# Kernel tuning notes

Hardware: AMD Instinct MI355X
Metric: run time of the kernel (lower is better)

The kernel has to match this reference:

```python
import jax, jax.numpy as jnp
import numpy as np

B, N, E, P, PH, H = 4, 512, 768, 64, 32, 8
D = E // H  # 96
FFN = 3072

def _ln(x, g, b, eps=1e-5):
    mu = jnp.mean(x, axis=-1, keepdims=True)
    var = jnp.mean((x - mu) ** 2, axis=-1, keepdims=True)
    return (x - mu) * jax.lax.rsqrt(var + eps) * g + b

def setup_inputs() -> dict:
    key = jax.random.key(0)
    ks = iter(jax.random.split(key, 80))
    def f(*s):
        return jax.random.normal(next(ks), s, jnp.float32) * 0.02
    ones = lambda *s: jnp.ones(s, jnp.float32)
    zeros = lambda *s: jnp.zeros(s, jnp.float32)
    return {
        'x': jax.random.normal(next(ks), (B, N, E), jnp.float32),
        'pair': jax.random.normal(next(ks), (B, N, N, P), jnp.float32) * 0.5,
        'attn_mask': zeros(B, 1, N, N),
        'op_mask': ones(B, N, 1),
        'op_norm': ones(1) / N,
        'nlist': jax.random.randint(next(ks), (B, N, 64), 0, N),
        'wq': f(E, E), 'wk': f(E, E), 'wv': f(E, E),
        'wg': f(E, E), 'bg': zeros(E),
        'wo': f(E, E), 'bo': zeros(E),
        'ln_pair_g': ones(P), 'ln_pair_b': zeros(P),
        'wb': f(H, P), 'bb': zeros(H),
        'ln_attn_g': ones(E), 'ln_attn_b': zeros(E),
        'ln_ffn_g': ones(E), 'ln_ffn_b': zeros(E),
        'w_ffn1': f(FFN, E), 'b_ffn1': zeros(FFN),
        'w_ffn2': f(E, FFN), 'b_ffn2': zeros(E),
        'ln_opm_g': ones(E), 'ln_opm_b': zeros(E),
        'w_opm_in': f(2 * PH, E), 'b_opm_in': zeros(2 * PH),
        'w_opm_out': f(P, PH * PH), 'b_opm_out': zeros(P),
        'ln_tm_g': ones(P), 'ln_tm_b': zeros(P),
        'w_tm_abp': f(2 * PH, P), 'b_tm_abp': zeros(2 * PH),
        'w_tm_abg': f(2 * PH, P), 'b_tm_abg': zeros(2 * PH),
        'w_tm_g': f(P, P), 'b_tm_g': zeros(P),
        'w_tm_z': f(P, PH), 'b_tm_z': zeros(P),
        'ln_tmo_g': ones(PH), 'ln_tmo_b': zeros(PH),
        'ln_pffn_g': ones(P), 'ln_pffn_b': zeros(P),
        'w_pffn1': f(P, P), 'b_pffn1': zeros(P),
        'w_pffn2': f(P, P), 'b_pffn2': zeros(P),
    }

def _forward(x, pair, attn_mask, op_mask, op_norm, wq, wk, wv, wg, bg, wo, bo,
             ln_pair_g, ln_pair_b, wb, bb, ln_attn_g, ln_attn_b,
             ln_ffn_g, ln_ffn_b, w_ffn1, b_ffn1, w_ffn2, b_ffn2,
             ln_opm_g, ln_opm_b, w_opm_in, b_opm_in, w_opm_out, b_opm_out,
             ln_tm_g, ln_tm_b, w_tm_abp, b_tm_abp, w_tm_abg, b_tm_abg,
             w_tm_g, b_tm_g, w_tm_z, b_tm_z, ln_tmo_g, ln_tmo_b,
             ln_pffn_g, ln_pffn_b, w_pffn1, b_pffn1, w_pffn2, b_pffn2):
    Bx, Nx, _ = x.shape
    # --- gated pair-bias self-attention (pre-LN, eval mode: dropout = identity) ---
    h = _ln(x, ln_attn_g, ln_attn_b)
    pn = _ln(pair, ln_pair_g, ln_pair_b)               # AtomAttention pair LayerNorm
    bias = jnp.einsum('bijp,hp->bhij', pn, wb) + bb[None, :, None, None]
    q = (h @ wq.T).reshape(Bx, Nx, H, D).transpose(0, 2, 1, 3) * (D ** -0.5)
    k = (h @ wk.T).reshape(Bx, Nx, H, D).transpose(0, 2, 1, 3)
    v = (h @ wv.T).reshape(Bx, Nx, H, D).transpose(0, 2, 1, 3)
    attn = jax.nn.softmax(jnp.einsum('bhid,bhjd->bhij', q, k) + attn_mask + bias, axis=-1)
    o = jnp.einsum('bhij,bhjd->bhid', attn, v).transpose(0, 2, 1, 3).reshape(Bx, Nx, E)
    o = jax.nn.sigmoid(h @ wg.T + bg) * o              # sigmoid output gate
    x = x + (o @ wo.T + bo)
    # --- atom transition MLP ---
    h = _ln(x, ln_ffn_g, ln_ffn_b)
    x = x + (jax.nn.gelu(h @ w_ffn1.T + b_ffn1, approximate=False) @ w_ffn2.T + b_ffn2)
    # --- OuterProduct pair update (fused: avoids [B,N,N,PH*PH] intermediate) ---
    h = _ln(x, ln_opm_g, ln_opm_b)
    ab = (h @ w_opm_in.T + b_opm_in) * op_mask
    a_o, b_o = jnp.split(ab, 2, axis=-1)               # each [B,N,PH]
    z = jnp.einsum('bid,bje,pde->bijp', a_o, b_o, w_opm_out.reshape(P, PH, PH)) + b_opm_out
    pair = pair + z * op_norm
    # --- triangle multiplication ---
    zp = _ln(pair, ln_tm_g, ln_tm_b)
    gpr = zp @ w_tm_g.T + b_tm_g                       # gate (no sigmoid, matches source)
    ab = (zp @ w_tm_abp.T + b_tm_abp) * jax.nn.sigmoid(zp @ w_tm_abg.T + b_tm_abg)
    a_t, b_t = jnp.split(ab, 2, axis=-1)               # each [B,N,N,PH]
    t = jnp.einsum('bijh,bkjh->bhik', a_t, b_t) + jnp.einsum('bjih,bjkh->bhik', a_t, b_t)
    t = _ln(t.transpose(0, 2, 3, 1), ln_tmo_g, ln_tmo_b) @ w_tm_z.T + b_tm_z
    pair = pair + gpr * t
    # --- pair transition MLP ---
    zp = _ln(pair, ln_pffn_g, ln_pffn_b)
    pair = pair + (jax.nn.gelu(zp @ w_pffn1.T + b_pffn1, approximate=False) @ w_pffn2.T + b_pffn2)
    return x, pair

def reference(x, pair, attn_mask, op_mask, op_norm, nlist, wq, wk, wv, wg, bg, wo, bo,
              ln_pair_g, ln_pair_b, wb, bb, ln_attn_g, ln_attn_b,
              ln_ffn_g, ln_ffn_b, w_ffn1, b_ffn1, w_ffn2, b_ffn2,
              ln_opm_g, ln_opm_b, w_opm_in, b_opm_in, w_opm_out, b_opm_out,
              ln_tm_g, ln_tm_b, w_tm_abp, b_tm_abp, w_tm_abg, b_tm_abg,
              w_tm_g, b_tm_g, w_tm_z, b_tm_z, ln_tmo_g, ln_tmo_b,
              ln_pffn_g, ln_pffn_b, w_pffn1, b_pffn1, w_pffn2, b_pffn2):
    del nlist  # accepted by the torch module but unused in the math
    return _forward(x, pair, attn_mask, op_mask, op_norm, wq, wk, wv, wg, bg, wo, bo,
                    ln_pair_g, ln_pair_b, wb, bb, ln_attn_g, ln_attn_b,
                    ln_ffn_g, ln_ffn_b, w_ffn1, b_ffn1, w_ffn2, b_ffn2,
                    ln_opm_g, ln_opm_b, w_opm_in, b_opm_in, w_opm_out, b_opm_out,
                    ln_tm_g, ln_tm_b, w_tm_abp, b_tm_abp, w_tm_abg, b_tm_abg,
                    w_tm_g, b_tm_g, w_tm_z, b_tm_z, ln_tmo_g, ln_tmo_b,
                    ln_pffn_g, ln_pffn_b, w_pffn1, b_pffn1, w_pffn2, b_pffn2)
```

## Files before the change

### kernel.cpp

```cpp
#include <hip/hip_runtime.h>
#include <hip/hip_bf16.h>
#include <math.h>

#define Nn 512
#define Ee 768
#define Pp 64
#define PHh 32
#define Hh 8
#define Dd 96
#define NNe 262144
#define LNEPS 1e-5f

typedef __attribute__((ext_vector_type(8))) short bf8;
typedef __attribute__((ext_vector_type(4))) short bf4;
typedef __attribute__((ext_vector_type(4))) float f32x4;
#define MFMA(a,b,c) __builtin_amdgcn_mfma_f32_16x16x32_bf16(a,b,c,0,0,0)

__device__ __forceinline__ short f2bf(float f) {
  __bf16 h = (__bf16)f;
  return __builtin_bit_cast(short, h);
}
__device__ __forceinline__ float bf2f(short s) {
  unsigned u = ((unsigned)(unsigned short)s) << 16;
  return __builtin_bit_cast(float, u);
}

__device__ __forceinline__ float wave_red_sum(float v) {
#pragma unroll
  for (int off = 32; off > 0; off >>= 1) v += __shfl_xor(v, off);
  return v;
}
__device__ __forceinline__ float gelu_exact(float v) {
  return 0.5f * v * (1.f + erff(v * 0.70710678118654752f));
}
__device__ __forceinline__ float sigmoidf_(float v) {
  return 1.f / (1.f + __expf(-v));
}
__device__ __forceinline__ float gelu_fast(float v) {
  return v / (1.f + __expf(-1.702f * v));
}

__global__ __launch_bounds__(256) void castw_kernel(
    const float* __restrict__ wq, const float* __restrict__ wk,
    const float* __restrict__ wv, const float* __restrict__ wg,
    const float* __restrict__ wo, const float* __restrict__ f1,
    const float* __restrict__ f2, const float* __restrict__ wop,
    const float* __restrict__ wb, const float* __restrict__ abp,
    const float* __restrict__ abg, const float* __restrict__ wtg,
    const float* __restrict__ wtz, const float* __restrict__ p1,
    const float* __restrict__ p2,
    short* __restrict__ dst, float qs) {
  long i = (long)blockIdx.x * 256 + threadIdx.x;
  float v;
  if (i < 589824) v = wq[i] * qs;
  else if (i < 1179648) v = wk[i - 589824];
  else if (i < 1769472) v = wv[i - 1179648];
  else if (i < 2359296) v = wg[i - 1769472];
  else if (i < 2949120) v = wo[i - 2359296];
  else if (i < 5308416) v = f1[i - 2949120];
  else if (i < 7667712) v = f2[i - 5308416];
  else if (i < 7716864) v = wop[i - 7667712];
  else if (i < 7717376) v = wb[i - 7716864];
  else if (i < 7721472) v = abp[i - 7717376];
  else if (i < 7725568) v = abg[i - 7721472];
  else if (i < 7729664) v = wtg[i - 7725568];
  else if (i < 7731712) v = wtz[i - 7729664];
  else if (i < 7735808) v = p1[i - 7731712];
  else if (i < 7739904) v = p2[i - 7735808];
  else return;
  dst[i] = f2bf(v);
}

__global__ __launch_bounds__(256) void ln_bf_kernel(const float* __restrict__ in,
                                                    short* __restrict__ out,
                                                    const float* __restrict__ gam,
                                                    const float* __restrict__ bet, int C) {
  int row = blockIdx.x;
  const float* xr = in + (long)row * C;
  short* yr = out + (long)row * C;
  float s = 0.f, ss = 0.f;
  for (int c = threadIdx.x; c < C; c += 256) { float v = xr[c]; s += v; ss += v * v; }
  s = wave_red_sum(s); ss = wave_red_sum(ss);
  __shared__ float sm[4][2];
  int wv = threadIdx.x >> 6, lane = threadIdx.x & 63;
  if (lane == 0) { sm[wv][0] = s; sm[wv][1] = ss; }
  __syncthreads();
  float ts = sm[0][0] + sm[1][0] + sm[2][0] + sm[3][0];
  float tss = sm[0][1] + sm[1][1] + sm[2][1] + sm[3][1];
  float mu = ts / C;
  float var = tss / C - mu * mu;
  float rs = rsqrtf(var + LNEPS);
  for (int c = threadIdx.x; c < C; c += 256) {
    float v = xr[c];
    yr[c] = f2bf((v - mu) * rs * gam[c] + bet[c]);
  }
}

__global__ __launch_bounds__(256) void gemm_bf(
    const short* __restrict__ A, int lda, long asB, long asH,
    const short* __restrict__ Bm, int ldb, long bsB, long bsH,
    float* __restrict__ outF, int ldf, long fsB, long fsH,
    short* __restrict__ outB, int ldob,
    const float* __restrict__ resid, int ldr, long rsB, long rsH,
    const float* __restrict__ bias,
    int M, int N, int K, int act, int vtrans, int Hdim) {
  int bz = blockIdx.z, bb = bz / Hdim, hh = bz % Hdim;
  A += bb * asB + hh * asH;
  Bm += bb * bsB + hh * bsH;
  if (outF) outF += bb * fsB + hh * fsH;
  if (outB) outB += bb * fsB + hh * fsH;
  if (resid) resid += bb * rsB + hh * rsH;
  __shared__ __align__(16) short As[64 * 72];
  __shared__ __align__(16) short Bs[64 * 72];
  int m0 = blockIdx.y * 64, n0 = blockIdx.x * 64;
  int tid = threadIdx.x;
  int wv = tid >> 6, lane = tid & 63;
  int wr = wv >> 1, wc = wv & 1;
  int lhi = lane >> 4, llo = lane & 15;
  int r4 = tid >> 2, c8 = (tid & 3) * 8;
  f32x4 acc[2][2] = {};
  for (int k0 = 0; k0 < K; k0 += 64) {
    *(bf8*)&As[r4 * 72 + c8] = *(const bf8*)(A + (long)(m0 + r4) * lda + k0 + c8);
    *(bf8*)&As[r4 * 72 + 32 + c8] =
        *(const bf8*)(A + (long)(m0 + r4) * lda + k0 + 32 + c8);
    bf8 bv0 = {}, bv1 = {};
    if (n0 + r4 < N) {
      bv0 = *(const bf8*)(Bm + (long)(n0 + r4) * ldb + k0 + c8);
      bv1 = *(const bf8*)(Bm + (long)(n0 + r4) * ldb + k0 + 32 + c8);
    }
    *(bf8*)&Bs[r4 * 72 + c8] = bv0;
    *(bf8*)&Bs[r4 * 72 + 32 + c8] = bv1;
    __syncthreads();
#pragma unroll
    for (int ks = 0; ks < 2; ++ks) {
      bf8 a0 = *(const bf8*)&As[(wr * 32 + llo) * 72 + ks * 32 + lhi * 8];
      bf8 a1 = *(const bf8*)&As[(wr * 32 + 16 + llo) * 72 + ks * 32 + lhi * 8];
      bf8 b0 = *(const bf8*)&Bs[(wc * 32 + llo) * 72 + ks * 32 + lhi * 8];
      bf8 b1 = *(const bf8*)&Bs[(wc * 32 + 16 + llo) * 72 + ks * 32 + lhi * 8];
      acc[0][0] = MFMA(a0, b0, acc[0][0]);
      acc[0][1] = MFMA(a0, b1, acc[0][1]);
      acc[1][0] = MFMA(a1, b0, acc[1][0]);
      acc[1][1] = MFMA(a1, b1, acc[1][1]);
    }
    __syncthreads();
  }
#pragma unroll
  for (int mi = 0; mi < 2; ++mi) {
    int gmb = m0 + wr * 32 + mi * 16 + lhi * 4;
#pragma unroll
    for (int ni = 0; ni < 2; ++ni) {
      int gn = n0 + wc * 32 + ni * 16 + llo;
      if (gn >= N) continue;
      float bv = bias ? bias[gn] : 0.f;
      float vr[4];
#pragma unroll
      for (int r = 0; r < 4; ++r) {
        float v = acc[mi][ni][r] + bv;
        if (resid) {
          float rv = resid[(long)(gmb + r) * ldr + gn];
          if (act == 2) v = sigmoidf_(rv) * acc[mi][ni][r];
          else v += rv;
        }
        if (act == 1) v = gelu_exact(v);
        vr[r] = v;
      }
      if (outF) {
#pragma unroll
        for (int r = 0; r < 4; ++r) outF[(long)(gmb + r) * ldf + gn] = vr[r];
      }
      if (outB) {
        if (vtrans) {
          bf4 pk;
#pragma unroll
          for (int r = 0; r < 4; ++r) pk[r] = f2bf(vr[r]);
          *(bf4*)(outB + ((long)((gmb >> 9) * 768 + gn) * 512 + (gmb & 511))) = pk;
        } else {
#pragma unroll
          for (int r = 0; r < 4; ++r) outB[(long)(gmb + r) * ldob + gn] = f2bf(vr[r]);
        }
      }
    }
  }
}

__global__ __launch_bounds__(256) void gemm_qkvg(
    const short* __restrict__ A, const short* __restrict__ W,
    short* __restrict__ q_bf, short* __restrict__ k_bf,
    short* __restrict__ vT_bf, float* __restrict__ gb,
    const float* __restrict__ bg) {
  __shared__ __align__(16) short As[128 * 40];
  __shared__ __align__(16) short Bs[128 * 40];
  int m0 = blockIdx.y * 128, n0 = blockIdx.x * 128;
// ... 393 lines not shown
#pragma unroll
    for (int mi = 0; mi < 2; ++mi)
#pragma unroll
      for (int r = 0; r < 4; ++r) { float v = x[mi][ni][r]; s += v; ss += v * v; }
    int e = wc * 32 + ni * 16 + llo;
    spS[grp][e][wr * 4 + lhi] = s;
    spQ[grp][e][wr * 4 + lhi] = ss;
  }
  __syncthreads();
  float mu1[2], rs1[2];
#pragma unroll
  for (int ni = 0; ni < 2; ++ni) {
    int e = wc * 32 + ni * 16 + llo;
    float s = 0.f, q2 = 0.f;
#pragma unroll
    for (int k = 0; k < 8; ++k) { s += spS[grp][e][k]; q2 += spQ[grp][e][k]; }
    float mu = s * 0.015625f, var = q2 * 0.015625f - mu * mu;
    mu1[ni] = mu; rs1[ni] = rsqrtf(var + LNEPS);
  }
#pragma unroll
  for (int mi = 0; mi < 2; ++mi) {
    f32x4 gv = *(const f32x4*)(gam + chb + mi * 16);
    f32x4 bv = *(const f32x4*)(bet + chb + mi * 16);
#pragma unroll
    for (int ni = 0; ni < 2; ++ni) {
      int e = wc * 32 + ni * 16 + llo;
      bf4 pk;
#pragma unroll
      for (int r = 0; r < 4; ++r)
        pk[r] = f2bf((x[mi][ni][r] - mu1[ni]) * rs1[ni] * gv[r] + bv[r]);
      *(bf4*)&Zb[grp][e * 72 + chb + mi * 16] = pk;
    }
  }
  __syncthreads();
  f32x4 ap[2][2] = {};
  f32x4 ag[2][2] = {};
#pragma unroll
  for (int ks = 0; ks < 2; ++ks) {
    bf8 z0 = *(const bf8*)&Zb[grp][(wr * 32 + llo) * 72 + ks * 32 + fc];
    bf8 z1 = *(const bf8*)&Zb[grp][(wr * 32 + 16 + llo) * 72 + ks * 32 + fc];
    bf8 p0 = *(const bf8*)&Wp[(wc * 32 + llo) * 72 + ks * 32 + fc];
    bf8 p1 = *(const bf8*)&Wp[(wc * 32 + 16 + llo) * 72 + ks * 32 + fc];
    bf8 g0 = *(const bf8*)&Wg[(wc * 32 + llo) * 72 + ks * 32 + fc];
    bf8 g1 = *(const bf8*)&Wg[(wc * 32 + 16 + llo) * 72 + ks * 32 + fc];
    ap[0][0] = MFMA(z0, p0, ap[0][0]);
    ap[0][1] = MFMA(z0, p1, ap[0][1]);
    ap[1][0] = MFMA(z1, p0, ap[1][0]);
    ap[1][1] = MFMA(z1, p1, ap[1][1]);
    ag[0][0] = MFMA(z0, g0, ag[0][0]);
    ag[0][1] = MFMA(z0, g1, ag[0][1]);
    ag[1][0] = MFMA(z1, g0, ag[1][0]);
    ag[1][1] = MFMA(z1, g1, ag[1][1]);
  }
#pragma unroll
  for (int mi = 0; mi < 2; ++mi) {
    int elemb = wr * 32 + mi * 16 + lhi * 4;
#pragma unroll
    for (int ni = 0; ni < 2; ++ni) {
      int ch = wc * 32 + ni * 16 + llo;
      float bp = b_abp[ch], bg = b_abg[ch];
      bf4 pack;
#pragma unroll
      for (int r = 0; r < 4; ++r)
        pack[r] = f2bf((ap[mi][ni][r] + bp) * sigmoidf_(ag[mi][ni][r] + bg));
      short* dst = (ch < 32) ? (aN + (long)ch * NNe) : (bN + (long)(ch - 32) * NNe);
      *(bf4*)(dst + ebase + elemb) = pack;
    }
  }
}

__global__ __launch_bounds__(512) void tm_tri_mfma(const short* __restrict__ aN4,
                                                   const short* __restrict__ bN4,
                                                   short* __restrict__ t4) {
  int lin = blockIdx.z * 16 + blockIdx.y * 4 + blockIdx.x;
  int vid = (lin & 7) * 256 + (lin >> 3);
  int hh = vid >> 4;
  int b = hh >> 5, h = hh & 31;
  int rem = vid & 15;
  int i0 = (rem >> 2) * 128, k0 = (rem & 3) * 128;
  const short* A = aN4 + (long)b * 8388608 + (long)h * NNe;
  const short* B = bN4 + (long)b * 8388608 + (long)h * NNe;
  __shared__ __align__(16) short A1[128 * 40];
  __shared__ __align__(16) short B1[128 * 40];
  __shared__ __align__(16) short A2[128 * 40];
  __shared__ __align__(16) short B2[128 * 40];
  int tid = threadIdx.x;
  int wv = tid >> 6, lane = tid & 63;
  int wr = wv >> 2, wc = wv & 3;
  int lhi = lane >> 4, llo = lane & 15;
  int r1 = tid >> 2, cp = (tid & 3) * 8;
  int s2 = tid >> 5, cg = (tid & 31) * 4;
  f32x4 acc[4][2] = {};
  for (int j0 = 0; j0 < 512; j0 += 32) {
    *(bf8*)&A1[r1 * 40 + cp] = *(const bf8*)(A + (long)(i0 + r1) * 512 + j0 + cp);
    *(bf8*)&B1[r1 * 40 + cp] = *(const bf8*)(B + (long)(k0 + r1) * 512 + j0 + cp);
    bf4 va0 = *(const bf4*)(A + (long)(j0 + 2 * s2) * 512 + i0 + cg);
    bf4 va1 = *(const bf4*)(A + (long)(j0 + 2 * s2 + 1) * 512 + i0 + cg);
    bf4 vb0 = *(const bf4*)(B + (long)(j0 + 2 * s2) * 512 + k0 + cg);
    bf4 vb1 = *(const bf4*)(B + (long)(j0 + 2 * s2 + 1) * 512 + k0 + cg);
#pragma unroll
    for (int q = 0; q < 4; ++q) {
      unsigned pa = (unsigned)(unsigned short)va0[q] |
                    ((unsigned)(unsigned short)va1[q] << 16);
      unsigned pb = (unsigned)(unsigned short)vb0[q] |
                    ((unsigned)(unsigned short)vb1[q] << 16);
      *(unsigned*)&A2[(cg + q) * 40 + 2 * s2] = pa;
      *(unsigned*)&B2[(cg + q) * 40 + 2 * s2] = pb;
    }
    __syncthreads();
    bf8 bfr[2], dfr[2];
#pragma unroll
    for (int ni = 0; ni < 2; ++ni) {
      bfr[ni] = *(const bf8*)&B1[(wc * 32 + ni * 16 + llo) * 40 + lhi * 8];
      dfr[ni] = *(const bf8*)&B2[(wc * 32 + ni * 16 + llo) * 40 + lhi * 8];
    }
#pragma unroll
    for (int mi = 0; mi < 4; ++mi) {
      bf8 a = *(const bf8*)&A1[(wr * 64 + mi * 16 + llo) * 40 + lhi * 8];
      acc[mi][0] = MFMA(a, bfr[0], acc[mi][0]);
      acc[mi][1] = MFMA(a, bfr[1], acc[mi][1]);
    }
#pragma unroll
    for (int mi = 0; mi < 4; ++mi) {
      bf8 c = *(const bf8*)&A2[(wr * 64 + mi * 16 + llo) * 40 + lhi * 8];
      acc[mi][0] = MFMA(c, dfr[0], acc[mi][0]);
      acc[mi][1] = MFMA(c, dfr[1], acc[mi][1]);
    }
    __syncthreads();
  }
  short* tp = t4 + (long)b * 8388608 + (long)h * NNe;
#pragma unroll
  for (int mi = 0; mi < 4; ++mi)
#pragma unroll
    for (int ni = 0; ni < 2; ++ni) {
      int row = i0 + wr * 64 + mi * 16 + lhi * 4;
      int col = k0 + wc * 32 + ni * 16 + llo;
#pragma unroll
      for (int r = 0; r < 4; ++r) tp[(long)(row + r) * 512 + col] = f2bf(acc[mi][ni][r]);
    }
}

__global__ __launch_bounds__(512) void upd_pffn_fused(
    const float* __restrict__ pin, float* __restrict__ pout,
    const short* __restrict__ t4,
    const short* __restrict__ Tb, const short* __restrict__ bo_bf,
    const float* __restrict__ b_out, const float* __restrict__ op_norm,
    const float* __restrict__ g_tm, const float* __restrict__ b_tm,
    const short* __restrict__ wg_a, const float* __restrict__ b_g,
    const short* __restrict__ wz_a, const float* __restrict__ b_z,
    const float* __restrict__ g_tmo, const float* __restrict__ b_tmo,
    const float* __restrict__ g_pf, const float* __restrict__ b_pf,
    const short* __restrict__ w1_a, const float* __restrict__ b1,
    const short* __restrict__ w2_a, const float* __restrict__ b2) {
  __shared__ __align__(16) short Zb[2][64 * 72];
  __shared__ __align__(16) short Tlb[2][64 * 40];
  __shared__ __align__(16) short Wbuf[64 * 72];
  __shared__ __align__(16) short Wzb[64 * 36];
  __shared__ float spS[2][64][9];
  __shared__ float spQ[2][64][9];
  __shared__ float spB[2][4][2][72];
  int tid = threadIdx.x;
  int grp = tid >> 8;
  int t = tid & 255;
  long e0 = (long)blockIdx.x * 128 + grp * 64;
  int bbt = (int)(e0 >> 18);
  long el = e0 & (NNe - 1);
  long growT = e0 >> 9;
  int jt = (int)((e0 >> 6) & 7);
  int wv = t >> 6, lane = t & 63;
  int wr = wv >> 1, wc = wv & 1;
  int lhi = lane >> 4, llo = lane & 15;
  int chb = wr * 32 + lhi * 4;
  int fc = lhi * 8;
  int fr0 = wr * 32 + llo, fr1 = fr0 + 16;
  int br0 = wc * 32 + llo, br1 = br0 + 16;
  int r0 = tid >> 3, c0 = (tid & 7) * 8;
  bf8 w1r, w2r;
  {
    *(bf8*)&Wbuf[r0 * 72 + c0] = *(const bf8*)(wg_a + r0 * 64 + c0);
    w1r = *(const bf8*)(w1_a + r0 * 64 + c0);
    w2r = *(const bf8*)(w2_a + r0 * 64 + c0);
    int rz = tid >> 3, cz = (tid & 7) * 4;
    *(bf4*)&Wzb[rz * 36 + cz] = *(const bf4*)(wz_a + rz * 32 + cz);
  }
  f32x4 x[2][2];
#pragma unroll
  for (int mi = 0; mi < 2; ++mi)
#pragma unroll
    for (int ni = 0; ni < 2; ++ni)
      x[mi][ni] = *(const f32x4*)(pin + (e0 + wc * 32 + ni * 16 + llo) * 64 +
                                  chb + mi * 16);
  {
    f32x4 acc[2][2] = {};
    bf8 a0 = *(const bf8*)(Tb + growT * 2048 + (long)fr0 * 32 + fc);
    bf8 a1 = *(const bf8*)(Tb + growT * 2048 + (long)fr1 * 32 + fc);
    bf8 b0 = *(const bf8*)(bo_bf + ((long)bbt * 512 + jt * 64 + br0) * 32 + fc);
    bf8 b1 = *(const bf8*)(bo_bf + ((long)bbt * 512 + jt * 64 + br1) * 32 + fc);
    acc[0][0] = MFMA(a0, b0, acc[0][0]);
    acc[0][1] = MFMA(a0, b1, acc[0][1]);
    acc[1][0] = MFMA(a1, b0, acc[1][0]);
    acc[1][1] = MFMA(a1, b1, acc[1][1]);
    float nrm = op_norm[0];
#pragma unroll
    for (int mi = 0; mi < 2; ++mi) {
      f32x4 bo4 = *(const f32x4*)(b_out + chb + mi * 16);
#pragma unroll
      for (int ni = 0; ni < 2; ++ni)
#pragma unroll
        for (int r = 0; r < 4; ++r)
          x[mi][ni][r] += (acc[mi][ni][r] + bo4[r]) * nrm;
    }
  }
#pragma unroll
  for (int ni = 0; ni < 2; ++ni) {
    float s = 0.f, ss = 0.f;
#pragma unroll
    for (int mi = 0; mi < 2; ++mi)
#pragma unroll
      for (int r = 0; r < 4; ++r) { float v = x[mi][ni][r]; s += v; ss += v * v; }
    int e = wc * 32 + ni * 16 + llo;
    spS[grp][e][wr * 4 + lhi] = s;
    spQ[grp][e][wr * 4 + lhi] = ss;
  }
  const short* t_in = t4 + (long)bbt * 8388608;
  int te = t & 63, tq = t >> 6;
  float tt[8];
  {
    float sB = 0.f, ssB = 0.f;
#pragma unroll
    for (int k = 0; k < 8; ++k) {
      float v = bf2f(t_in[(long)(tq * 8 + k) * NNe + el + te]);
      tt[k] = v; sB += v; ssB += v * v;
    }
    spB[grp][tq][0][te] = sB; spB[grp][tq][1][te] = ssB;
  }
  __syncthreads();
  {
    float ts = spB[grp][0][0][te] + spB[grp][1][0][te] + spB[grp][2][0][te] +
               spB[grp][3][0][te];
    float tss = spB[grp][0][1][te] + spB[grp][1][1][te] + spB[grp][2][1][te] +
                spB[grp][3][1][te];
    float mu = ts * 0.03125f, var = tss * 0.03125f - mu * mu;
    float rs = rsqrtf(var + LNEPS);
    bf8 pk;
#pragma unroll
    for (int k = 0; k < 8; ++k) {
      int c = tq * 8 + k;
      pk[k] = f2bf((tt[k] - mu) * rs * g_tmo[c] + b_tmo[c]);
    }
    *(bf8*)&Tlb[grp][te * 40 + tq * 8] = pk;
  }
  float mu1[2], rs1[2];
#pragma unroll
  for (int ni = 0; ni < 2; ++ni) {
    int e = wc * 32 + ni * 16 + llo;
    float s = 0.f, q2 = 0.f;
#pragma unroll
    for (int k = 0; k < 8; ++k) { s += spS[grp][e][k]; q2 += spQ[grp][e][k]; }
    float mu = s * 0.015625f, var = q2 * 0.015625f - mu * mu;
    mu1[ni] = mu; rs1[ni] = rsqrtf(var + LNEPS);
  }
#pragma unroll
  for (int mi = 0; mi < 2; ++mi) {
    f32x4 gv = *(const f32x4*)(g_tm + chb + mi * 16);
    f32x4 bv = *(const f32x4*)(b_tm + chb + mi * 16);
#pragma unroll
    for (int ni = 0; ni < 2; ++ni) {
      int e = wc * 32 + ni * 16 + llo;
      bf4 pk;
#pragma unroll
      for (int r = 0; r < 4; ++r)
        pk[r] = f2bf((x[mi][ni][r] - mu1[ni]) * rs1[ni] * gv[r] + bv[r]);
      *(bf4*)&Zb[grp][e * 72 + chb + mi * 16] = pk;
    }
  }
  __syncthreads();
  f32x4 accg[2][2] = {};
  f32x4 accz[2][2] = {};
#pragma unroll
  for (int ks = 0; ks < 2; ++ks) {
    bf8 a0 = *(const bf8*)&Wbuf[fr0 * 72 + ks * 32 + fc];
    bf8 a1 = *(const bf8*)&Wbuf[fr1 * 72 + ks * 32 + fc];
    bf8 z0 = *(const bf8*)&Zb[grp][br0 * 72 + ks * 32 + fc];
    bf8 z1 = *(const bf8*)&Zb[grp][br1 * 72 + ks * 32 + fc];
    accg[0][0] = MFMA(a0, z0, accg[0][0]);
    accg[0][1] = MFMA(a0, z1, accg[0][1]);
    accg[1][0] = MFMA(a1, z0, accg[1][0]);
    accg[1][1] = MFMA(a1, z1, accg[1][1]);
  }
  {
    bf8 a0 = *(const bf8*)&Wzb[fr0 * 36 + fc];
    bf8 a1 = *(const bf8*)&Wzb[fr1 * 36 + fc];
    bf8 t0 = *(const bf8*)&Tlb[grp][br0 * 40 + fc];
    bf8 t1 = *(const bf8*)&Tlb[grp][br1 * 40 + fc];
    accz[0][0] = MFMA(a0, t0, accz[0][0]);
    accz[0][1] = MFMA(a0, t1, accz[0][1]);
    accz[1][0] = MFMA(a1, t0, accz[1][0]);
    accz[1][1] = MFMA(a1, t1, accz[1][1]);
  }
#pragma unroll
  for (int mi = 0; mi < 2; ++mi) {
    f32x4 bgv = *(const f32x4*)(b_g + chb + mi * 16);
    f32x4 bzv = *(const f32x4*)(b_z + chb + mi * 16);
#pragma unroll
    for (int ni = 0; ni < 2; ++ni)
#pragma unroll
      for (int r = 0; r < 4; ++r)
        x[mi][ni][r] += (accg[mi][ni][r] + bgv[r]) * (accz[mi][ni][r] + bzv[r]);
  }
#pragma unroll
  for (int ni = 0; ni < 2; ++ni) {
    float s = 0.f, ss = 0.f;
#pragma unroll
    for (int mi = 0; mi < 2; ++mi)
#pragma unroll
      for (int r = 0; r < 4; ++r) { float v = x[mi][ni][r]; s += v; ss += v * v; }
    int e = wc * 32 + ni * 16 + llo;
    spS[grp][e][wr * 4 + lhi] = s;
    spQ[grp][e][wr * 4 + lhi] = ss;
  }
  __syncthreads();
  *(bf8*)&Wbuf[r0 * 72 + c0] = w1r;
#pragma unroll
  for (int ni = 0; ni < 2; ++ni) {
    int e = wc * 32 + ni * 16 + llo;
    float s = 0.f, q2 = 0.f;
#pragma unroll
    for (int k = 0; k < 8; ++k) { s += spS[grp][e][k]; q2 += spQ[grp][e][k]; }
    float mu = s * 0.015625f, var = q2 * 0.015625f - mu * mu;
    mu1[ni] = mu; rs1[ni] = rsqrtf(var + LNEPS);
  }
#pragma unroll
  for (int mi = 0; mi < 2; ++mi) {
    f32x4 gv = *(const f32x4*)(g_pf + chb + mi * 16);
    f32x4 bv = *(const f32x4*)(b_pf + chb + mi * 16);
#pragma unroll
    for (int ni = 0; ni < 2; ++ni) {
      int e = wc * 32 + ni * 16 + llo;
      bf4 pk;
#pragma unroll
      for (int r = 0; r < 4; ++r)
        pk[r] = f2bf((x[mi][ni][r] - mu1[ni]) * rs1[ni] * gv[r] + bv[r]);
      *(bf4*)&Zb[grp][e * 72 + chb + mi * 16] = pk;
    }
  }
  __syncthreads();
  f32x4 acc1[2][2] = {};
#pragma unroll
  for (int ks = 0; ks < 2; ++ks) {
    bf8 a0 = *(const bf8*)&Wbuf[fr0 * 72 + ks * 32 + fc];
    bf8 a1 = *(const bf8*)&Wbuf[fr1 * 72 + ks * 32 + fc];
    bf8 z0 = *(const bf8*)&Zb[grp][br0 * 72 + ks * 32 + fc];
    bf8 z1 = *(const bf8*)&Zb[grp][br1 * 72 + ks * 32 + fc];
    acc1[0][0] = MFMA(a0, z0, acc1[0][0]);
    acc1[0][1] = MFMA(a0, z1, acc1[0][1]);
    acc1[1][0] = MFMA(a1, z0, acc1[1][0]);
    acc1[1][1] = MFMA(a1, z1, acc1[1][1]);
  }
  __syncthreads();
  *(bf8*)&Wbuf[r0 * 72 + c0] = w2r;
#pragma unroll
  for (int mi = 0; mi < 2; ++mi) {
    f32x4 bv = *(const f32x4*)(b1 + chb + mi * 16);
#pragma unroll
    for (int ni = 0; ni < 2; ++ni) {
      int e = wc * 32 + ni * 16 + llo;
      bf4 pk;
#pragma unroll
      for (int r = 0; r < 4; ++r) pk[r] = f2bf(gelu_fast(acc1[mi][ni][r] + bv[r]));
      *(bf4*)&Zb[grp][e * 72 + chb + mi * 16] = pk;
    }
  }
  __syncthreads();
  f32x4 acc2[2][2] = {};
#pragma unroll
  for (int ks = 0; ks < 2; ++ks) {
    bf8 a0 = *(const bf8*)&Wbuf[fr0 * 72 + ks * 32 + fc];
    bf8 a1 = *(const bf8*)&Wbuf[fr1 * 72 + ks * 32 + fc];
    bf8 z0 = *(const bf8*)&Zb[grp][br0 * 72 + ks * 32 + fc];
    bf8 z1 = *(const bf8*)&Zb[grp][br1 * 72 + ks * 32 + fc];
    acc2[0][0] = MFMA(a0, z0, acc2[0][0]);
    acc2[0][1] = MFMA(a0, z1, acc2[0][1]);
    acc2[1][0] = MFMA(a1, z0, acc2[1][0]);
    acc2[1][1] = MFMA(a1, z1, acc2[1][1]);
  }
#pragma unroll
  for (int mi = 0; mi < 2; ++mi) {
    f32x4 bv = *(const f32x4*)(b2 + chb + mi * 16);
#pragma unroll
    for (int ni = 0; ni < 2; ++ni) {
#pragma unroll
      for (int r = 0; r < 4; ++r) x[mi][ni][r] += acc2[mi][ni][r] + bv[r];
      *(f32x4*)(pout + (e0 + wc * 32 + ni * 16 + llo) * 64 + chb + mi * 16) =
          x[mi][ni];
    }
  }
}

extern "C" void kernel_launch(void* const* d_in, const int* in_sizes, int n_in,
                              void* d_out, int out_size, void* d_ws, size_t ws_size,
                              hipStream_t stream) {
  const float* x = (const float*)d_in[0];
  const float* pair = (const float*)d_in[1];
  const float* attn_mask = (const float*)d_in[2];
  const float* op_mask = (const float*)d_in[3];
  const float* op_norm = (const float*)d_in[4];
  const float* wq = (const float*)d_in[6];
  const float* wk = (const float*)d_in[7];
  const float* wv_ = (const float*)d_in[8];
  const float* wg = (const float*)d_in[9];
  const float* bg = (const float*)d_in[10];
  const float* wo = (const float*)d_in[11];
  const float* bo = (const float*)d_in[12];
  const float* ln_pair_g = (const float*)d_in[13];
  const float* ln_pair_b = (const float*)d_in[14];
  const float* wb = (const float*)d_in[15];
  const float* bb = (const float*)d_in[16];
  const float* ln_attn_g = (const float*)d_in[17];
  const float* ln_attn_b = (const float*)d_in[18];
  const float* ln_ffn_g = (const float*)d_in[19];
  const float* ln_ffn_b = (const float*)d_in[20];
  const float* w_ffn1 = (const float*)d_in[21];
  const float* b_ffn1 = (const float*)d_in[22];
  const float* w_ffn2 = (const float*)d_in[23];
  const float* b_ffn2 = (const float*)d_in[24];
  const float* ln_opm_g = (const float*)d_in[25];
  const float* ln_opm_b = (const float*)d_in[26];
  const float* w_opm_in = (const float*)d_in[27];
  const float* b_opm_in = (const float*)d_in[28];
  const float* w_opm_out = (const float*)d_in[29];
  const float* b_opm_out = (const float*)d_in[30];
  const float* ln_tm_g = (const float*)d_in[31];
  const float* ln_tm_b = (const float*)d_in[32];
  const float* w_tm_abp = (const float*)d_in[33];
  const float* b_tm_abp = (const float*)d_in[34];
  const float* w_tm_abg = (const float*)d_in[35];
  const float* b_tm_abg = (const float*)d_in[36];
  const float* w_tm_g = (const float*)d_in[37];
  const float* b_tm_g = (const float*)d_in[38];
  const float* w_tm_z = (const float*)d_in[39];
  const float* b_tm_z = (const float*)d_in[40];
  const float* ln_tmo_g = (const float*)d_in[41];
  const float* ln_tmo_b = (const float*)d_in[42];
  const float* ln_pffn_g = (const float*)d_in[43];
  const float* ln_pffn_b = (const float*)d_in[44];
  const float* w_pffn1 = (const float*)d_in[45];
  const float* b_pffn1 = (const float*)d_in[46];
  const float* w_pffn2 = (const float*)d_in[47];
  const float* b_pffn2 = (const float*)d_in[48];

  float* ws = (float*)d_ws;
  short* wbf = (short*)ws;
  short* wq_bf = wbf + 0;
  short* wo_bf = wbf + 2359296;
  short* wf1_bf = wbf + 2949120;
  short* wf2_bf = wbf + 5308416;
  short* wop_bf = wbf + 7667712;
  short* wb_a = wbf + 7716864;
  short* wabp_a = wbf + 7717376;
  short* wabg_a = wbf + 7721472;
  short* wtg_a = wbf + 7725568;
  short* wtz_a = wbf + 7729664;
  short* wp1_a = wbf + 7731712;
  short* wp2_a = wbf + 7735808;

  short* h_bf = (short*)(ws + 3869952);
  short* q_bf = (short*)(ws + 4656384);
  short* k_bf = (short*)(ws + 5442816);
  short* vT_bf = (short*)(ws + 6229248);
  float* gb = ws + 7015680;
  short* gb_bf = (short*)(ws + 10161408);
  float* x1b = ws + 10947840;
  short* biasb_bf = (short*)(ws + 12520704);
  short* attn_bf = (short*)(ws + 16715008);
  short* mffn_bf = (short*)(ws + 20909312);
  float* abb = ws + 24055040;
  short* abb_bf = (short*)(ws + 24186112);
  short* Tb_bf = (short*)(ws + 24218880);
  short* aN4 = (short*)(ws + 59870464);
  short* bN4 = (short*)(ws + 76647680);
  short* t4 = (short*)(ws + 93424896);

  float* xo = (float*)d_out;
  float* pair1 = xo + 1572864;

  const float qscale = 0.1020620726159658f;

  castw_kernel<<<30234, 256, 0, stream>>>(wq, wk, wv_, wg, wo, w_ffn1, w_ffn2, w_opm_in,
                                          wb, w_tm_abp, w_tm_abg, w_tm_g, w_tm_z,
                                          w_pffn1, w_pffn2, wbf, qscale);
  ln_bf_kernel<<<2048, 256, 0, stream>>>(x, h_bf, ln_attn_g, ln_attn_b, 768);
  gemm_qkvg<<<dim3(24, 16, 1), 256, 0, stream>>>(h_bf, wq_bf, q_bf, k_bf, vT_bf, gb, bg);
  pair_bias_mfma<<<8192, 512, 0, stream>>>(pair, ln_pair_g, ln_pair_b, wb_a, bb, biasb_bf);
  attn_fused<<<dim3(32, 8, 4), 256, 0, stream>>>(q_bf, k_bf, biasb_bf, attn_mask, attn_bf);
  gemm_bf<<<dim3(2, 8, 32), 256, 0, stream>>>(attn_bf, 512, 2097152, 262144,
                                              vT_bf, 512, 393216, 49152,
                                              nullptr, 0, 393216, 96, gb_bf, 768,
                                              gb, 768, 393216, 96, nullptr,
                                              512, 96, 512, 2, 0, 8);
  gemm128<<<dim3(6, 16, 1), 256, 0, stream>>>(gb_bf, wo_bf, 768, x, bo, x1b);
  ln_bf_kernel<<<2048, 256, 0, stream>>>(x1b, h_bf, ln_ffn_g, ln_ffn_b, 768);
  gemm_ffn1<<<dim3(24, 16, 1), 256, 0, stream>>>(h_bf, wf1_bf, mffn_bf, b_ffn1);
  gemm128<<<dim3(6, 16, 1), 256, 0, stream>>>(mffn_bf, wf2_bf, 3072, x1b, b_ffn2, xo);
  ln_bf_kernel<<<2048, 256, 0, stream>>>(xo, h_bf, ln_opm_g, ln_opm_b, 768);
  gemm_bf<<<dim3(1, 32, 1), 256, 0, stream>>>(h_bf, 768, 0, 0, wop_bf, 768, 0, 0,
                                              abb, 64, 0, 0, nullptr, 0,
                                              nullptr, 0, 0, 0, b_opm_in,
                                              2048, 64, 768, 0, 0, 1);
  opmask_kernel<<<512, 256, 0, stream>>>(abb, op_mask, abb_bf);
  opm_T_kernel<<<dim3(256, 64, 1), dim3(32, 8, 1), 0, stream>>>(abb, w_opm_out, Tb_bf);
  opm_ab_fused<<<dim3(4, 512, 4), 512, 0, stream>>>(
      pair, Tb_bf, abb_bf, b_opm_out, op_norm,
      ln_tm_g, ln_tm_b, wabp_a, b_tm_abp, wabg_a, b_tm_abg, aN4, bN4);
  tm_tri_mfma<<<dim3(4, 4, 128), 512, 0, stream>>>(aN4, bN4, t4);
  upd_pffn_fused<<<8192, 512, 0, stream>>>(
      pair, pair1, t4, Tb_bf, abb_bf, b_opm_out, op_norm,
      ln_tm_g, ln_tm_b, wtg_a, b_tm_g, wtz_a, b_tm_z,
      ln_tmo_g, ln_tmo_b, ln_pffn_g, ln_pffn_b, wp1_a, b_pffn1, wp2_a, b_pffn2);
}
```

Baseline: 867.0 us.

## Restructure pair update kernel so each wave owns 16 edges and skips block barriers

```diff
diff --git a/kernel.cpp b/kernel.cpp
--- a/kernel.cpp
+++ b/kernel.cpp
@@ -38,6 +38,10 @@
 }
 __device__ __forceinline__ float gelu_fast(float v) {
   return v / (1.f + __expf(-1.702f * v));
+}
+__device__ __forceinline__ void wave_fence() {
+  asm volatile("s_waitcnt lgkmcnt(0)" ::: "memory");
+  __builtin_amdgcn_sched_barrier(0);
 }
 
 __global__ __launch_bounds__(256) void castw_kernel(
@@ -737,248 +741,170 @@
     const float* __restrict__ g_pf, const float* __restrict__ b_pf,
     const short* __restrict__ w1_a, const float* __restrict__ b1,
     const short* __restrict__ w2_a, const float* __restrict__ b2) {
-  __shared__ __align__(16) short Zb[2][64 * 72];
-  __shared__ __align__(16) short Tlb[2][64 * 40];
-  __shared__ __align__(16) short Wbuf[64 * 72];
-  __shared__ __align__(16) short Wzb[64 * 36];
-  __shared__ float spS[2][64][9];
-  __shared__ float spQ[2][64][9];
-  __shared__ float spB[2][4][2][72];
+  __shared__ __align__(16) short Wg[64 * 72];
+  __shared__ __align__(16) short Wz[64 * 36];
+  __shared__ __align__(16) short W1s[64 * 72];
+  __shared__ __align__(16) short W2s[64 * 72];
+  __shared__ __align__(16) short Zw[8][16 * 72];
   int tid = threadIdx.x;
-  int grp = tid >> 8;
-  int t = tid & 255;
-  long e0 = (long)blockIdx.x * 128 + grp * 64;
+  int wid = tid >> 6, lane = tid & 63;
+  int llo = lane & 15, lhi = lane >> 4;
+  long e0 = (long)blockIdx.x * 128;
   int bbt = (int)(e0 >> 18);
-  long el = e0 & (NNe - 1);
+  long el = (e0 & (NNe - 1)) + wid * 16 + llo;
+  long elG = e0 + wid * 16 + llo;
   long growT = e0 >> 9;
-  int jt = (int)((e0 >> 6) & 7);
-  int wv = t >> 6, lane = t & 63;
-  int wr = wv >> 1, wc = wv & 1;
-  int lhi = lane >> 4, llo = lane & 15;
-  int chb = wr * 32 + lhi * 4;
-  int fc = lhi * 8;
-  int fr0 = wr * 32 + llo, fr1 = fr0 + 16;
-  int br0 = wc * 32 + llo, br1 = br0 + 16;
-  int r0 = tid >> 3, c0 = (tid & 7) * 8;
-  bf8 w1r, w2r;
+  int jcol = (int)(el & 511);
   {
-    *(bf8*)&Wbuf[r0 * 72 + c0] = *(const bf8*)(wg_a + r0 * 64 + c0);
-    w1r = *(const bf8*)(w1_a + r0 * 64 + c0);
-    w2r = *(const bf8*)(w2_a + r0 * 64 + c0);
-    int rz = tid >> 3, cz = (tid & 7) * 4;
-    *(bf4*)&Wzb[rz * 36 + cz] = *(const bf4*)(wz_a + rz * 32 + cz);
-  }
-  f32x4 x[2][2];
-#pragma unroll
-  for (int mi = 0; mi < 2; ++mi)
-#pragma unroll
-    for (int ni = 0; ni < 2; ++ni)
-      x[mi][ni] = *(const f32x4*)(pin + (e0 + wc * 32 + ni * 16 + llo) * 64 +
-                                  chb + mi * 16);
+    int r0 = tid >> 3, c0 = (tid & 7) * 8, cz = (tid & 7) * 4;
+    *(bf8*)&Wg[r0 * 72 + c0] = *(const bf8*)(wg_a + r0 * 64 + c0);
+    *(bf8*)&W1s[r0 * 72 + c0] = *(const bf8*)(w1_a + r0 * 64 + c0);
+    *(bf8*)&W2s[r0 * 72 + c0] = *(const bf8*)(w2_a + r0 * 64 + c0);
+    *(bf4*)&Wz[r0 * 36 + cz] = *(const bf4*)(wz_a + r0 * 32 + cz);
+  }
+  short* zb = &Zw[wid][0];
+  f32x4 x[4];
+#pragma unroll
+  for (int mo = 0; mo < 4; ++mo)
+    x[mo] = *(const f32x4*)(pin + elG * 64 + mo * 16 + lhi * 4);
+  const short* t_in = t4 + (long)bbt * 8388608;
+  float tt[8];
+#pragma unroll
+  for (int k = 0; k < 8; ++k)
+    tt[k] = bf2f(t_in[(long)(lhi * 8 + k) * NNe + el]);
   {
-    f32x4 acc[2][2] = {};
-    bf8 a0 = *(const bf8*)(Tb + growT * 2048 + (long)fr0 * 32 + fc);
-    bf8 a1 = *(const bf8*)(Tb + growT * 2048 + (long)fr1 * 32 + fc);
-    bf8 b0 = *(const bf8*)(bo_bf + ((long)bbt * 512 + jt * 64 + br0) * 32 + fc);
-    bf8 b1 = *(const bf8*)(bo_bf + ((long)bbt * 512 + jt * 64 + br1) * 32 + fc);
-    acc[0][0] = MFMA(a0, b0, acc[0][0]);
-    acc[0][1] = MFMA(a0, b1, acc[0][1]);
-    acc[1][0] = MFMA(a1, b0, acc[1][0]);
-    acc[1][1] = MFMA(a1, b1, acc[1][1]);
+    bf8 bo_f = *(const bf8*)(bo_bf + ((long)bbt * 512 + jcol) * 32 + lhi * 8);
     float nrm = op_norm[0];
 #pragma unroll
-    for (int mi = 0; mi < 2; ++mi) {
-      f32x4 bo4 = *(const f32x4*)(b_out + chb + mi * 16);
-#pragma unroll
-      for (int ni = 0; ni < 2; ++ni)
-#pragma unroll
-        for (int r = 0; r < 4; ++r)
-          x[mi][ni][r] += (acc[mi][ni][r] + bo4[r]) * nrm;
-    }
-  }
-#pragma unroll
-  for (int ni = 0; ni < 2; ++ni) {
+    for (int mo = 0; mo < 4; ++mo) {
+      bf8 a = *(const bf8*)(Tb + growT * 2048 + (long)(mo * 16 + llo) * 32 + lhi * 8);
+      f32x4 acc = {0.f, 0.f, 0.f, 0.f};
+      acc = MFMA(a, bo_f, acc);
+      f32x4 bo4 = *(const f32x4*)(b_out + mo * 16 + lhi * 4);
+#pragma unroll
+      for (int r = 0; r < 4; ++r) x[mo][r] += (acc[r] + bo4[r]) * nrm;
+    }
+  }
+  {
     float s = 0.f, ss = 0.f;
 #pragma unroll
-    for (int mi = 0; mi < 2; ++mi)
-#pragma unroll
-      for (int r = 0; r < 4; ++r) { float v = x[mi][ni][r]; s += v; ss += v * v; }
-    int e = wc * 32 + ni * 16 + llo;
-    spS[grp][e][wr * 4 + lhi] = s;
-    spQ[grp][e][wr * 4 + lhi] = ss;
-  }
-  const short* t_in = t4 + (long)bbt * 8388608;
-  int te = t & 63, tq = t >> 6;
-  float tt[8];
+    for (int mo = 0; mo < 4; ++mo)
+#pragma unroll
+      for (int r = 0; r < 4; ++r) { float v = x[mo][r]; s += v; ss += v * v; }
+    s += __shfl_xor(s, 16); s += __shfl_xor(s, 32);
+    ss += __shfl_xor(ss, 16); ss += __shfl_xor(ss, 32);
+    float mu = s * 0.015625f, var = ss * 0.015625f - mu * mu;
+    float rs = rsqrtf(var + LNEPS);
+#pragma unroll
+    for (int mo = 0; mo < 4; ++mo) {
+      f32x4 gv = *(const f32x4*)(g_tm + mo * 16 + lhi * 4);
+      f32x4 bv = *(const f32x4*)(b_tm + mo * 16 + lhi * 4);
+      bf4 pk;
+#pragma unroll
+      for (int r = 0; r < 4; ++r)
+        pk[r] = f2bf((x[mo][r] - mu) * rs * gv[r] + bv[r]);
+      *(bf4*)&zb[llo * 72 + mo * 16 + lhi * 4] = pk;
+    }
+  }
+  __syncthreads();
+  f32x4 accg[4] = {};
+#pragma unroll
+  for (int ks = 0; ks < 2; ++ks) {
+    bf8 zf = *(const bf8*)&zb[llo * 72 + ks * 32 + lhi * 8];
+#pragma unroll
+    for (int mo = 0; mo < 4; ++mo) {
+      bf8 a = *(const bf8*)&Wg[(mo * 16 + llo) * 72 + ks * 32 + lhi * 8];
+      accg[mo] = MFMA(a, zf, accg[mo]);
+    }
+  }
+  f32x4 accz[4] = {};
   {
-    float sB = 0.f, ssB = 0.f;
+    float s = 0.f, ss = 0.f;
+#pragma unroll
+    for (int k = 0; k < 8; ++k) { s += tt[k]; ss += tt[k] * tt[k]; }
+    s += __shfl_xor(s, 16); s += __shfl_xor(s, 32);
+    ss += __shfl_xor(ss, 16); ss += __shfl_xor(ss, 32);
+    float mu = s * 0.03125f, var = ss * 0.03125f - mu * mu;
+    float rs = rsqrtf(var + LNEPS);
+    bf8 tf;
 #pragma unroll
     for (int k = 0; k < 8; ++k) {
-      float v = bf2f(t_in[(long)(tq * 8 + k) * NNe + el + te]);
-      tt[k] = v; sB += v; ssB += v * v;
-    }
-    spB[grp][tq][0][te] = sB; spB[grp][tq][1][te] = ssB;
-  }
-  __syncthreads();
+      int c = lhi * 8 + k;
+      tf[k] = f2bf((tt[k] - mu) * rs * g_tmo[c] + b_tmo[c]);
+    }
+#pragma unroll
+    for (int mo = 0; mo < 4; ++mo) {
+      bf8 a = *(const bf8*)&Wz[(mo * 16 + llo) * 36 + lhi * 8];
+      accz[mo] = MFMA(a, tf, accz[mo]);
+    }
+  }
+#pragma unroll
+  for (int mo = 0; mo < 4; ++mo) {
+    f32x4 bgv = *(const f32x4*)(b_g + mo * 16 + lhi * 4);
+    f32x4 bzv = *(const f32x4*)(b_z + mo * 16 + lhi * 4);
+#pragma unroll
+    for (int r = 0; r < 4; ++r)
+      x[mo][r] += (accg[mo][r] + bgv[r]) * (accz[mo][r] + bzv[r]);
+  }
   {
-    float ts = spB[grp][0][0][te] + spB[grp][1][0][te] + spB[grp][2][0][te] +
-               spB[grp][3][0][te];
-    float tss = spB[grp][0][1][te] + spB[grp][1][1][te] + spB[grp][2][1][te] +
-                spB[grp][3][1][te];
-    float mu = ts * 0.03125f, var = tss * 0.03125f - mu * mu;
+    float s = 0.f, ss = 0.f;
+#pragma unroll
+    for (int mo = 0; mo < 4; ++mo)
+#pragma unroll
+      for (int r = 0; r < 4; ++r) { float v = x[mo][r]; s += v; ss += v * v; }
+    s += __shfl_xor(s, 16); s += __shfl_xor(s, 32);
+    ss += __shfl_xor(ss, 16); ss += __shfl_xor(ss, 32);
+    float mu = s * 0.015625f, var = ss * 0.015625f - mu * mu;
     float rs = rsqrtf(var + LNEPS);
-    bf8 pk;
-#pragma unroll
-    for (int k = 0; k < 8; ++k) {
-      int c = tq * 8 + k;
-      pk[k] = f2bf((tt[k] - mu) * rs * g_tmo[c] + b_tmo[c]);
-    }
-    *(bf8*)&Tlb[grp][te * 40 + tq * 8] = pk;
-  }
-  float mu1[2], rs1[2];
-#pragma unroll
-  for (int ni = 0; ni < 2; ++ni) {
-    int e = wc * 32 + ni * 16 + llo;
-    float s = 0.f, q2 = 0.f;
-#pragma unroll
-    for (int k = 0; k < 8; ++k) { s += spS[grp][e][k]; q2 += spQ[grp][e][k]; }
-    float mu = s * 0.015625f, var = q2 * 0.015625f - mu * mu;
-    mu1[ni] = mu; rs1[ni] = rsqrtf(var + LNEPS);
-  }
-#pragma unroll
-  for (int mi = 0; mi < 2; ++mi) {
-    f32x4 gv = *(const f32x4*)(g_tm + chb + mi * 16);
-    f32x4 bv = *(const f32x4*)(b_tm + chb + mi * 16);
-#pragma unroll
-    for (int ni = 0; ni < 2; ++ni) {
-      int e = wc * 32 + ni * 16 + llo;
+    wave_fence();
+#pragma unroll
+    for (int mo = 0; mo < 4; ++mo) {
+      f32x4 gv = *(const f32x4*)(g_pf + mo * 16 + lhi * 4);
+      f32x4 bv = *(const f32x4*)(b_pf + mo * 16 + lhi * 4);
       bf4 pk;
 #pragma unroll
       for (int r = 0; r < 4; ++r)
-        pk[r] = f2bf((x[mi][ni][r] - mu1[ni]) * rs1[ni] * gv[r] + bv[r]);
-      *(bf4*)&Zb[grp][e * 72 + chb + mi * 16] = pk;
-    }
-  }
-  __syncthreads();
-  f32x4 accg[2][2] = {};
-  f32x4 accz[2][2] = {};
+        pk[r] = f2bf((x[mo][r] - mu) * rs * gv[r] + bv[r]);
+      *(bf4*)&zb[llo * 72 + mo * 16 + lhi * 4] = pk;
+    }
+  }
+  wave_fence();
+  f32x4 acc1[4] = {};
 #pragma unroll
   for (int ks = 0; ks < 2; ++ks) {
-    bf8 a0 = *(const bf8*)&Wbuf[fr0 * 72 + ks * 32 + fc];
-    bf8 a1 = *(const bf8*)&Wbuf[fr1 * 72 + ks * 32 + fc];
-    bf8 z0 = *(const bf8*)&Zb[grp][br0 * 72 + ks * 32 + fc];
-    bf8 z1 = *(const bf8*)&Zb[grp][br1 * 72 + ks * 32 + fc];
-    accg[0][0] = MFMA(a0, z0, accg[0][0]);
-    accg[0][1] = MFMA(a0, z1, accg[0][1]);
-    accg[1][0] = MFMA(a1, z0, accg[1][0]);
-    accg[1][1] = MFMA(a1, z1, accg[1][1]);
-  }
-  {
-    bf8 a0 = *(const bf8*)&Wzb[fr0 * 36 + fc];
-    bf8 a1 = *(const bf8*)&Wzb[fr1 * 36 + fc];
-    bf8 t0 = *(const bf8*)&Tlb[grp][br0 * 40 + fc];
-    bf8 t1 = *(const bf8*)&Tlb[grp][br1 * 40 + fc];
-    accz[0][0] = MFMA(a0, t0, accz[0][0]);
-    accz[0][1] = MFMA(a0, t1, accz[0][1]);
-    accz[1][0] = MFMA(a1, t0, accz[1][0]);
-    accz[1][1] = MFMA(a1, t1, accz[1][1]);
-  }
-#pragma unroll
-  for (int mi = 0; mi < 2; ++mi) {
-    f32x4 bgv = *(const f32x4*)(b_g + chb + mi * 16);
-    f32x4 bzv = *(const f32x4*)(b_z + chb + mi * 16);
-#pragma unroll
-    for (int ni = 0; ni < 2; ++ni)
-#pragma unroll
-      for (int r = 0; r < 4; ++r)
-        x[mi][ni][r] += (accg[mi][ni][r] + bgv[r]) * (accz[mi][ni][r] + bzv[r]);
-  }
-#pragma unroll
-  for (int ni = 0; ni < 2; ++ni) {
-    float s = 0.f, ss = 0.f;
-#pragma unroll
-    for (int mi = 0; mi < 2; ++mi)
-#pragma unroll
-      for (int r = 0; r < 4; ++r) { float v = x[mi][ni][r]; s += v; ss += v * v; }
-    int e = wc * 32 + ni * 16 + llo;
-    spS[grp][e][wr * 4 + lhi] = s;
-    spQ[grp][e][wr * 4 + lhi] = ss;
-  }
-  __syncthreads();
-  *(bf8*)&Wbuf[r0 * 72 + c0] = w1r;
-#pragma unroll
-  for (int ni = 0; ni < 2; ++ni) {
-    int e = wc * 32 + ni * 16 + llo;
-    float s = 0.f, q2 = 0.f;
-#pragma unroll
-    for (int k = 0; k < 8; ++k) { s += spS[grp][e][k]; q2 += spQ[grp][e][k]; }
-    float mu = s * 0.015625f, var = q2 * 0.015625f - mu * mu;
-    mu1[ni] = mu; rs1[ni] = rsqrtf(var + LNEPS);
-  }
-#pragma unroll
-  for (int mi = 0; mi < 2; ++mi) {
-    f32x4 gv = *(const f32x4*)(g_pf + chb + mi * 16);
-    f32x4 bv = *(const f32x4*)(b_pf + chb + mi * 16);
-#pragma unroll
-    for (int ni = 0; ni < 2; ++ni) {
-      int e = wc * 32 + ni * 16 + llo;
-      bf4 pk;
-#pragma unroll
-      for (int r = 0; r < 4; ++r)
-        pk[r] = f2bf((x[mi][ni][r] - mu1[ni]) * rs1[ni] * gv[r] + bv[r]);
-      *(bf4*)&Zb[grp][e * 72 + chb + mi * 16] = pk;
-    }
-  }
-  __syncthreads();
-  f32x4 acc1[2][2] = {};
+    bf8 zf = *(const bf8*)&zb[llo * 72 + ks * 32 + lhi * 8];
+#pragma unroll
+    for (int mo = 0; mo < 4; ++mo) {
+      bf8 a = *(const bf8*)&W1s[(mo * 16 + llo) * 72 + ks * 32 + lhi * 8];
+      acc1[mo] = MFMA(a, zf, acc1[mo]);
+    }
+  }
+  wave_fence();
+#pragma unroll
+  for (int mo = 0; mo < 4; ++mo) {
+    f32x4 bv = *(const f32x4*)(b1 + mo * 16 + lhi * 4);
+    bf4 pk;
+#pragma unroll
+    for (int r = 0; r < 4; ++r) pk[r] = f2bf(gelu_fast(acc1[mo][r] + bv[r]));
+    *(bf4*)&zb[llo * 72 + mo * 16 + lhi * 4] = pk;
+  }
+  wave_fence();
+  f32x4 acc2[4] = {};
 #pragma unroll
   for (int ks = 0; ks < 2; ++ks) {
-    bf8 a0 = *(const bf8*)&Wbuf[fr0 * 72 + ks * 32 + fc];
-    bf8 a1 = *(const bf8*)&Wbuf[fr1 * 72 + ks * 32 + fc];
-    bf8 z0 = *(const bf8*)&Zb[grp][br0 * 72 + ks * 32 + fc];
-    bf8 z1 = *(const bf8*)&Zb[grp][br1 * 72 + ks * 32 + fc];
-    acc1[0][0] = MFMA(a0, z0, acc1[0][0]);
-    acc1[0][1] = MFMA(a0, z1, acc1[0][1]);
-    acc1[1][0] = MFMA(a1, z0, acc1[1][0]);
-    acc1[1][1] = MFMA(a1, z1, acc1[1][1]);
-  }
-  __syncthreads();
-  *(bf8*)&Wbuf[r0 * 72 + c0] = w2r;
-#pragma unroll
-  for (int mi = 0; mi < 2; ++mi) {
-    f32x4 bv = *(const f32x4*)(b1 + chb + mi * 16);
-#pragma unroll
-    for (int ni = 0; ni < 2; ++ni) {
-      int e = wc * 32 + ni * 16 + llo;
-      bf4 pk;
-#pragma unroll
-      for (int r = 0; r < 4; ++r) pk[r] = f2bf(gelu_fast(acc1[mi][ni][r] + bv[r]));
-      *(bf4*)&Zb[grp][e * 72 + chb + mi * 16] = pk;
-    }
-  }
-  __syncthreads();
-  f32x4 acc2[2][2] = {};
-#pragma unroll
-  for (int ks = 0; ks < 2; ++ks) {
-    bf8 a0 = *(const bf8*)&Wbuf[fr0 * 72 + ks * 32 + fc];
-    bf8 a1 = *(const bf8*)&Wbuf[fr1 * 72 + ks * 32 + fc];
-    bf8 z0 = *(const bf8*)&Zb[grp][br0 * 72 + ks * 32 + fc];
-    bf8 z1 = *(const bf8*)&Zb[grp][br1 * 72 + ks * 32 + fc];
-    acc2[0][0] = MFMA(a0, z0, acc2[0][0]);
-    acc2[0][1] = MFMA(a0, z1, acc2[0][1]);
-    acc2[1][0] = MFMA(a1, z0, acc2[1][0]);
-    acc2[1][1] = MFMA(a1, z1, acc2[1][1]);
-  }
-#pragma unroll
-  for (int mi = 0; mi < 2; ++mi) {
-    f32x4 bv = *(const f32x4*)(b2 + chb + mi * 16);
-#pragma unroll
-    for (int ni = 0; ni < 2; ++ni) {
-#pragma unroll
-      for (int r = 0; r < 4; ++r) x[mi][ni][r] += acc2[mi][ni][r] + bv[r];
-      *(f32x4*)(pout + (e0 + wc * 32 + ni * 16 + llo) * 64 + chb + mi * 16) =
-          x[mi][ni];
-    }
+    bf8 zf = *(const bf8*)&zb[llo * 72 + ks * 32 + lhi * 8];
+#pragma unroll
+    for (int mo = 0; mo < 4; ++mo) {
+      bf8 a = *(const bf8*)&W2s[(mo * 16 + llo) * 72 + ks * 32 + lhi * 8];
+      acc2[mo] = MFMA(a, zf, acc2[mo]);
+    }
+  }
+#pragma unroll
+  for (int mo = 0; mo < 4; ++mo) {
+    f32x4 bv = *(const f32x4*)(b2 + mo * 16 + lhi * 4);
+#pragma unroll
+    for (int r = 0; r < 4; ++r) x[mo][r] += acc2[mo][r] + bv[r];
+    *(f32x4*)(pout + elG * 64 + mo * 16 + lhi * 4) = x[mo];
   }
 }
 
```

New measurement: 871.8 us. Within noise of the previous version (+0.5%).
